# Optimization experiments

Measured on AMD Instinct MI355X. Metric: run time of the kernel, lower is better.

## Reference

```python
import jax, jax.numpy as jnp
import numpy as np

HIDDEN = 1024
MOE_INTER = 512
SHARED_INTER = 2048
N_EXPERTS = 32
TOP_K = 6
N_GROUP = 8
TOPK_GROUP = 4
ROUTED_SCALE = 2.5


def setup_inputs() -> dict:
    key = jax.random.key(0)
    ks = jax.random.split(key, 6)
    s = 0.02
    return {
        "hidden_states": jax.random.normal(ks[0], (2, 1024, HIDDEN), jnp.float32),
        "gate_w": jax.random.normal(ks[1], (N_EXPERTS, HIDDEN), jnp.float32) * s,
        "e_bias": jnp.zeros((N_EXPERTS,), jnp.float32),  # e_score_correction_bias (non-trainable)
        "up_w": jax.random.normal(ks[2], (N_EXPERTS, MOE_INTER, HIDDEN), jnp.float32) * s,
        "down_w": jax.random.normal(ks[3], (N_EXPERTS, HIDDEN, MOE_INTER), jnp.float32) * s,
        "shared_up_w": jax.random.normal(ks[4], (SHARED_INTER, HIDDEN), jnp.float32) * s,
        "shared_down_w": jax.random.normal(ks[5], (HIDDEN, SHARED_INTER), jnp.float32) * s,
    }


def _relu2(x):
    # Nemotron-H 'relu2' activation: relu(x)^2
    return jnp.square(jax.nn.relu(x))


def _router(x, gate_w, e_bias):
    # x: [T, H] -> topk_idx [T, K] (int), topk_w [T, K] (fp32)
    T = x.shape[0]
    logits = x.astype(jnp.float32) @ gate_w.astype(jnp.float32).T  # [T, E]
    scores = jax.nn.sigmoid(logits)
    sc = scores + e_bias[None, :]
    # group-limited routing: top-2 sum per group, keep topk_group groups
    g = sc.reshape(T, N_GROUP, N_EXPERTS // N_GROUP)
    group_scores = jax.lax.top_k(g, 2)[0].sum(-1)                  # [T, G]
    group_idx = jax.lax.top_k(group_scores, TOPK_GROUP)[1]         # [T, TG]
    group_mask = jnp.zeros_like(group_scores).at[jnp.arange(T)[:, None], group_idx].set(1.0)
    score_mask = jnp.repeat(group_mask, N_EXPERTS // N_GROUP, axis=1)  # [T, E]
    masked = jnp.where(score_mask > 0, sc, 0.0)
    topk_idx = jax.lax.stop_gradient(jax.lax.top_k(masked, TOP_K)[1])  # torch path is @no_grad
    topk_w = jnp.take_along_axis(scores, topk_idx, axis=1)         # gather from unbiased scores
    topk_w = topk_w / (topk_w.sum(-1, keepdims=True) + 1e-20)      # norm_topk_prob
    topk_w = topk_w * ROUTED_SCALE
    return topk_idx, topk_w


def reference(hidden_states, gate_w, e_bias, up_w, down_w, shared_up_w, shared_down_w):
    B, S, H = hidden_states.shape
    x = hidden_states.reshape(-1, H)  # [T, H]
    T = x.shape[0]
    topk_idx, topk_w = _router(x, gate_w, e_bias)
    # combine weights as dense [T, E] (scatter of top-k weights)
    combine = jnp.zeros((T, N_EXPERTS), topk_w.dtype).at[jnp.arange(T)[:, None], topk_idx].add(topk_w)
    # dense-masked expert compute; weight applied on intermediate (equivalent since
    # down_proj is linear with no bias): out = sum_e w_te * down_e(act(up_e(x)))
    h = _relu2(jnp.einsum('th,eih->tei', x, up_w))   # [T, E, I]
    h = h * combine[:, :, None]
    moe_out = jnp.einsum('tei,ehi->th', h, down_w)   # [T, H]
    shared = _relu2(x @ shared_up_w.T) @ shared_down_w.T
    return (moe_out + shared).reshape(B, S, H)


if __name__ == "__main__":
    out = reference(**setup_inputs())
    print(out.shape, out.dtype)
```

## Files before the change

### kernel.cpp

```cpp
#include <hip/hip_runtime.h>

typedef unsigned short u16;
typedef __bf16 bf16x8 __attribute__((ext_vector_type(8)));
typedef float f32x4 __attribute__((ext_vector_type(4)));
typedef u16 u16x8 __attribute__((ext_vector_type(8)));

#define T_TOK 2048
#define HID   1024
#define NEXP  32
#define IM    512
#define SI    2048
#define TOPK  6
#define PLAN_MAX 160

__device__ __forceinline__ u16 f2bf(float f){
  unsigned u = __float_as_uint(f);
  u += 0x7FFFu + ((u >> 16) & 1u);
  return (u16)(u >> 16);
}

__device__ __forceinline__ void gll16(const void* g, void* l){
  __builtin_amdgcn_global_load_lds((const __attribute__((address_space(1))) void*)g,
                                   (__attribute__((address_space(3))) void*)l, 16, 0, 0);
}

__device__ __forceinline__ u16x8 cvt2(float4 a, float4 b){
  u16x8 o;
  o[0] = f2bf(a.x); o[1] = f2bf(a.y); o[2] = f2bf(a.z); o[3] = f2bf(a.w);
  o[4] = f2bf(b.x); o[5] = f2bf(b.y); o[6] = f2bf(b.z); o[7] = f2bf(b.w);
  return o;
}

__global__ __launch_bounds__(256) void cvt_big_kernel(const float4* __restrict__ s1,
                                                      const float4* __restrict__ s2,
                                                      u16x8* __restrict__ d1,
                                                      u16x8* __restrict__ d2){
  long i = (long)blockIdx.x * 256 + threadIdx.x;
  const float4* s; u16x8* d;
  if (i < 2097152L){ s = s1; d = d1; }
  else             { s = s2; d = d2; i -= 2097152L; }
  float4 a = s[2*i], b = s[2*i+1];
  d[i] = cvt2(a, b);
}

__global__ __launch_bounds__(256) void cvt_small_router_kernel(
    const float* __restrict__ x, const float4* __restrict__ s3, const float4* __restrict__ s4,
    const float* __restrict__ gate, const float* __restrict__ ebias,
    u16x8* __restrict__ d0, u16x8* __restrict__ d3, u16x8* __restrict__ d4,
    int* __restrict__ ce, float* __restrict__ cw){
  int blk = blockIdx.x;
  if (blk >= 512){
    long i = (long)(blk - 512) * 256 + threadIdx.x;
    const float4* s; u16x8* d;
    if      (i < 262144L){ s = (const float4*)x; d = d0; }
    else if (i < 524288L){ s = s3; d = d3; i -= 262144L; }
    else                 { s = s4; d = d4; i -= 524288L; }
    float4 a = s[2*i], b = s[2*i+1];
    d[i] = cvt2(a, b);
    return;
  }
  int wave = threadIdx.x >> 6;
  int lane = threadIdx.x & 63;
  int t = blk * 4 + wave;
  int e = lane & 31, half = lane >> 5;
  const float4* xv = (const float4*)(x + (size_t)t * HID);
  const float4* gv = (const float4*)(gate + (size_t)e * HID);
  double d0a = 0, d1a = 0, d2a = 0, d3a = 0;
  for (int i = half * 128; i < half * 128 + 128; i++){
    float4 a = xv[i], b = gv[i];
    d0a += (double)a.x * b.x; d1a += (double)a.y * b.y;
    d2a += (double)a.z * b.z; d3a += (double)a.w * b.w;
  }
  double acc = (d0a + d1a) + (d2a + d3a);
  acc += __shfl_xor(acc, 32);
  double score = 1.0 / (1.0 + exp(-acc));
  double sc = score + (double)ebias[e];
  double o1  = __shfl_xor(sc, 1);
  double hi  = fmax(sc, o1), lo = fmin(sc, o1);
  double ohi = __shfl_xor(hi, 2), olo = __shfl_xor(lo, 2);
  double gs  = (hi >= ohi) ? hi + fmax(lo, ohi) : ohi + fmax(olo, hi);
  int g = e >> 2;
  int rank = 0;
#pragma unroll
  for (int j = 0; j < 8; j++){
    double gj = __shfl(gs, j * 4);
    if (gj > gs || (gj == gs && j < g)) rank++;
  }
  double cur = (rank < 4) ? sc : 0.0;
  int sel_e[TOPK]; double sel_w[TOPK]; double wsum = 0.0;
#pragma unroll
  for (int k = 0; k < TOPK; k++){
    double bv = cur; int bi = lane;
#pragma unroll
    for (int m = 32; m >= 1; m >>= 1){
      double ov = __shfl_xor(bv, m); int oi = __shfl_xor(bi, m);
      if (ov > bv || (ov == bv && oi < bi)) { bv = ov; bi = oi; }
    }
    if ((bi & 31) == e) cur = -1e300;
    double ws = __shfl(score, bi);
    sel_e[k] = bi; sel_w[k] = ws; wsum += ws;
  }
  double scale = 2.5 / (wsum + 1e-20);
#pragma unroll
  for (int k = 0; k < TOPK; k++){
    if (lane == k){
      ce[t * TOPK + k] = sel_e[k] & 31;
      cw[t * TOPK + k] = (float)(sel_w[k] * scale);
    }
  }
}

__global__ __launch_bounds__(256) void build_kernel(const int* __restrict__ ce,
                                                    const float* __restrict__ cw,
                                                    int* __restrict__ cnt,
                                                    int* __restrict__ tok,
                                                    float* __restrict__ wl){
  int e = blockIdx.x;
  int tid = threadIdx.x, lane = tid & 63, wave = tid >> 6;
  __shared__ int wsum[4];
  int running = 0;
  for (int base = 0; base < T_TOK * TOPK; base += 256){
    int i = base + tid;
    bool m = (ce[i] == e);
    unsigned long long bal = __ballot(m);
    int woff = __popcll(bal & ((1ull << lane) - 1ull));
    if (lane == 0) wsum[wave] = __popcll(bal);
    __syncthreads();
    int wbase = 0;
#pragma unroll
    for (int wv = 0; wv < 4; wv++) if (wv < wave) wbase += wsum[wv];
    int btot = wsum[0] + wsum[1] + wsum[2] + wsum[3];
    if (m){
      int t = i / TOPK, k = i - t * TOPK;
      int pos = running + wbase + woff;
      tok[e * T_TOK + pos] = (t << 3) | k;
      wl[e * T_TOK + pos] = cw[i];
    }
    running += btot;
    __syncthreads();
  }
  if (tid == 0) cnt[e] = running;
}

__global__ __launch_bounds__(256) void plan_kernel(const int* __restrict__ cnt,
                                                   int* __restrict__ plan){
  int tid = threadIdx.x;
  if (tid < PLAN_MAX) plan[1 + tid] = -1;
  __syncthreads();
  if (tid == 0){
    int n = 0;
    for (int e = 0; e < NEXP; e++){
      int c = cnt[e];
      for (int tb = 0; tb < c; tb += 128) plan[1 + n++] = (tb << 8) | e;
    }
    plan[0] = n;
  }
}

__device__ __forceinline__ void gemm_core(
    const char* gA0, const char* gA1, const char* gB0, const char* gB1,
    u16* lA, u16* lB, int iters, int tid, int wrow, int wcol, int quad, int l16,
    f32x4 acc[4][4])
{
  char* bA = (char*)lA + tid*16;
  char* bB = (char*)lB + tid*16;
  gll16(gA0, bA);  gll16(gA1, bA + 4096);
  gll16(gB0, bB);  gll16(gB1, bB + 4096);
  gA0 += 64; gA1 += 64; gB0 += 64; gB1 += 64;
  __syncthreads();
  unsigned cur = 0;
  for (int it = 0; it < iters - 1; ++it){
    unsigned nxt = cur ^ 1;
    gll16(gA0, bA + nxt*8192);  gll16(gA1, bA + nxt*8192 + 4096);
    gll16(gB0, bB + nxt*8192);  gll16(gB1, bB + nxt*8192 + 4096);
    gA0 += 64; gA1 += 64; gB0 += 64; gB1 += 64;
    const u16* rA = lA + cur*4096;
    const u16* rB = lB + cur*4096;
    bf16x8 af[4], bfr[4];
#pragma unroll
    for (int mt = 0; mt < 4; mt++) af[mt]  = *(const bf16x8*)&rA[(wrow + mt*16 + l16)*32 + quad*8];
#pragma unroll
    for (int nt = 0; nt < 4; nt++) bfr[nt] = *(const bf16x8*)&rB[(wcol + nt*16 + l16)*32 + quad*8];
#pragma unroll
    for (int mt = 0; mt < 4; mt++)
#pragma unroll
      for (int nt = 0; nt < 4; nt++)
        acc[mt][nt] = __builtin_amdgcn_mfma_f32_16x16x32_bf16(af[mt], bfr[nt], acc[mt][nt], 0, 0, 0);
    __syncthreads();
    cur = nxt;
  }
  const u16* rA = lA + cur*4096;
  const u16* rB = lB + cur*4096;
  bf16x8 af[4], bfr[4];
#pragma unroll
  for (int mt = 0; mt < 4; mt++) af[mt]  = *(const bf16x8*)&rA[(wrow + mt*16 + l16)*32 + quad*8];
#pragma unroll
  for (int nt = 0; nt < 4; nt++) bfr[nt] = *(const bf16x8*)&rB[(wcol + nt*16 + l16)*32 + quad*8];
#pragma unroll
  for (int mt = 0; mt < 4; mt++)
#pragma unroll
    for (int nt = 0; nt < 4; nt++)
      acc[mt][nt] = __builtin_amdgcn_mfma_f32_16x16x32_bf16(af[mt], bfr[nt], acc[mt][nt], 0, 0, 0);
}

#define ACC_INIT f32x4 acc[4][4]; \
  _Pragma("unroll") for (int i_ = 0; i_ < 4; i_++) \
  _Pragma("unroll") for (int j_ = 0; j_ < 4; j_++) acc[i_][j_] = (f32x4){0.f,0.f,0.f,0.f};

__global__ __launch_bounds__(256) void up_fused_kernel(
    const u16* __restrict__ xb, const u16* __restrict__ supb, const u16* __restrict__ upb,
    const int* __restrict__ cnt, const int* __restrict__ tok, const float* __restrict__ wl,
    const int* __restrict__ plan, u16* __restrict__ shh, u16* __restrict__ hws){
  __shared__ u16 lA[2*128*32], lB[2*128*32];
  int tid = threadIdx.x;
  int lane = tid & 63, wave = tid >> 6, quad = lane >> 4, l16 = lane & 15;
  int wrow = (wave >> 1)*64, wcol = (wave & 1)*64;
  int srow = tid >> 2, sseg = (tid & 3)*16;
  int blk = blockIdx.x;
  if (blk < 256){
    int bm = (blk >> 4) * 128, bn = (blk & 15) * 128;
    const char* gA0 = (const char*)(xb + (size_t)(bm + srow)*HID) + sseg;
    const char* gA1 = (const char*)(xb + (size_t)(bm + 64 + srow)*HID) + sseg;
    const char* gB0 = (const char*)(supb + (size_t)(bn + srow)*HID) + sseg;
    const char* gB1 = (const char*)(supb + (size_t)(bn + 64 + srow)*HID) + sseg;
    ACC_INIT;
    gemm_core(gA0, gA1, gB0, gB1, lA, lB, HID/32, tid, wrow, wcol, quad, l16, acc);
#pragma unroll
    for (int mt = 0; mt < 4; mt++)
#pragma unroll
      for (int nt = 0; nt < 4; nt++)
#pragma unroll
        for (int r = 0; r < 4; r++){
          int m = bm + wrow + mt*16 + quad*4 + r;
          int n = bn + wcol + nt*16 + l16;
          float v = acc[mt][nt][r]; v = fmaxf(v, 0.f); v *= v;
          shh[(size_t)m*SI + n] = f2bf(v);
        }
  } else {
    int eu = blk - 256;
    int pv = plan[1 + (eu >> 2)];
    if (pv < 0) return;
    int e = pv & 255;
    int tb = pv >> 8;
    int c = cnt[e];
    int bn = (eu & 3) * 128;
    const int* tl = tok + e * T_TOK;
    const float* wle = wl + e * T_TOK;
    int s0 = tb + srow;      if (s0 > c-1) s0 = c-1;
    int s1 = tb + 64 + srow; if (s1 > c-1) s1 = c-1;
    int t0 = tl[s0] >> 3, t1 = tl[s1] >> 3;
    const char* gA0 = (const char*)(xb + (size_t)t0*HID) + sseg;
    const char* gA1 = (const char*)(xb + (size_t)t1*HID) + sseg;
    const u16* Bb = upb + (size_t)e * IM * HID;
    const char* gB0 = (const char*)(Bb + (size_t)(bn + srow)*HID) + sseg;
    const char* gB1 = (const char*)(Bb + (size_t)(bn + 64 + srow)*HID) + sseg;
    ACC_INIT;
    gemm_core(gA0, gA1, gB0, gB1, lA, lB, HID/32, tid, wrow, wcol, quad, l16, acc);
#pragma unroll
    for (int mt = 0; mt < 4; mt++)
#pragma unroll
      for (int r = 0; r < 4; r++){
        int s = tb + wrow + mt*16 + quad*4 + r;
        if (s < c){
          int code = tl[s];
          float w = wle[s];
          size_t hb = ((size_t)(code >> 3) * TOPK + (code & 7)) * IM;
#pragma unroll
          for (int nt = 0; nt < 4; nt++){
            float v = acc[mt][nt][r]; v = fmaxf(v, 0.f); v = v * v * w;
            hws[hb + bn + wcol + nt*16 + l16] = f2bf(v);
          }
        }
      }
  }
}

__global__ __launch_bounds__(256) void down_fused_kernel(
    const u16* __restrict__ shh, const u16* __restrict__ sdnb,
    const u16* __restrict__ hws, const u16* __restrict__ dnb,
    const int* __restrict__ cnt, const int* __restrict__ tok, const int* __restrict__ plan,
    float* __restrict__ out){
  __shared__ u16 lA[2*128*32], lB[2*128*32];
  int tid = threadIdx.x;
  int lane = tid & 63, wave = tid >> 6, quad = lane >> 4, l16 = lane & 15;
  int wrow = (wave >> 1)*64, wcol = (wave & 1)*64;
  int srow = tid >> 2, sseg = (tid & 3)*16;
  int blk = blockIdx.x;
  if (blk < 128){
    int bm = (blk >> 3)*128, bn = (blk & 7)*128;
    const char* gA0 = (const char*)(shh + (size_t)(bm + srow)*SI) + sseg;
    const char* gA1 = (const char*)(shh + (size_t)(bm + 64 + srow)*SI) + sseg;
    const char* gB0 = (const char*)(sdnb + (size_t)(bn + srow)*SI) + sseg;
    const char* gB1 = (const char*)(sdnb + (size_t)(bn + 64 + srow)*SI) + sseg;
    ACC_INIT;
    gemm_core(gA0, gA1, gB0, gB1, lA, lB, SI/32, tid, wrow, wcol, quad, l16, acc);
#pragma unroll
    for (int mt = 0; mt < 4; mt++)
#pragma unroll
      for (int nt = 0; nt < 4; nt++)
#pragma unroll
        for (int r = 0; r < 4; r++){
          int m = bm + wrow + mt*16 + quad*4 + r;
          int n = bn + wcol + nt*16 + l16;
          unsafeAtomicAdd(&out[(size_t)m*HID + n], acc[mt][nt][r]);
        }
  } else {
    int eu = blk - 128;
    int pv = plan[1 + (eu >> 3)];
    if (pv < 0) return;
    int e = pv & 255;
    int tb = pv >> 8;
    int c = cnt[e];
    int bn = (eu & 7) * 128;
    const int* tl = tok + e * T_TOK;
    int s0 = tb + srow;      if (s0 > c-1) s0 = c-1;
    int s1 = tb + 64 + srow; if (s1 > c-1) s1 = c-1;
    int c0 = tl[s0], c1 = tl[s1];
    const char* gA0 = (const char*)(hws + ((size_t)(c0 >> 3)*TOPK + (c0 & 7))*IM) + sseg;
    const char* gA1 = (const char*)(hws + ((size_t)(c1 >> 3)*TOPK + (c1 & 7))*IM) + sseg;
    const u16* Bb = dnb + (size_t)e * HID * IM;
    const char* gB0 = (const char*)(Bb + (size_t)(bn + srow)*IM) + sseg;
    const char* gB1 = (const char*)(Bb + (size_t)(bn + 64 + srow)*IM) + sseg;
    ACC_INIT;
    gemm_core(gA0, gA1, gB0, gB1, lA, lB, IM/32, tid, wrow, wcol, quad, l16, acc);
#pragma unroll
    for (int mt = 0; mt < 4; mt++)
#pragma unroll
      for (int r = 0; r < 4; r++){
        int s = tb + wrow + mt*16 + quad*4 + r;
        if (s < c){
          int code = tl[s];
          float* ob = out + (size_t)(code >> 3) * HID;
#pragma unroll
          for (int nt = 0; nt < 4; nt++)
            unsafeAtomicAdd(&ob[bn + wcol + nt*16 + l16], acc[mt][nt][r]);
        }
      }
  }
}

extern "C" void kernel_launch(void* const* d_in, const int* in_sizes, int n_in,
                              void* d_out, int out_size, void* d_ws, size_t ws_size,
                              hipStream_t stream) {
  const float* x    = (const float*)d_in[0];
  const float* gate = (const float*)d_in[1];
  const float* eb   = (const float*)d_in[2];
  const float* upw  = (const float*)d_in[3];
  const float* dnw  = (const float*)d_in[4];
  const float* supw = (const float*)d_in[5];
  const float* sdnw = (const float*)d_in[6];
  float* out = (float*)d_out;

  char* w = (char*)d_ws;
  size_t o = 0;
  int*   cnt  = (int*)(w + o);   o += 1024;
  int*   plan = (int*)(w + o);   o += 1024;
  int*   ce   = (int*)(w + o);   o += (size_t)T_TOK * TOPK * 4;
  float* cw   = (float*)(w + o); o += (size_t)T_TOK * TOPK * 4;
  int*   tok  = (int*)(w + o);   o += (size_t)NEXP * T_TOK * 4;
  float* wl   = (float*)(w + o); o += (size_t)NEXP * T_TOK * 4;
  u16*   xb   = (u16*)(w + o);   o += (size_t)T_TOK * HID * 2;
  u16*   dnb  = (u16*)(w + o);   o += (size_t)NEXP * HID * IM * 2;
  u16*   hws  = (u16*)(w + o);   o += (size_t)T_TOK * TOPK * IM * 2;
  u16*   upb  = (u16*)(w + o);   o += (size_t)NEXP * IM * HID * 2;
  u16*   supb = (u16*)(w + o);   o += (size_t)SI * HID * 2;
  u16*   sdnb = (u16*)(w + o);   o += (size_t)HID * SI * 2;
  u16*   shh  = (u16*)(w + o);   o += (size_t)T_TOK * SI * 2;

  cvt_big_kernel<<<16384, 256, 0, stream>>>(
      (const float4*)upw, (const float4*)dnw, (u16x8*)upb, (u16x8*)dnb);
  cvt_small_router_kernel<<<3584, 256, 0, stream>>>(
      x, (const float4*)supw, (const float4*)sdnw, gate, eb,
      (u16x8*)xb, (u16x8*)supb, (u16x8*)sdnb, ce, cw);
  build_kernel<<<NEXP, 256, 0, stream>>>(ce, cw, cnt, tok, wl);
  plan_kernel<<<1, 256, 0, stream>>>(cnt, plan);

  up_fused_kernel<<<896, 256, 0, stream>>>(xb, supb, upb, cnt, tok, wl, plan, shh, hws);
  hipMemsetAsync(out, 0, (size_t)T_TOK * HID * 4, stream);
  down_fused_kernel<<<1408, 256, 0, stream>>>(shh, sdnb, hws, dnb, cnt, tok, plan, out);
}
```

Measured before the change: 369.6 us.

## Merge prep kernels, fold plan into build, swizzle LDS, split-K shared down GEMM

```diff
diff --git a/kernel.cpp b/kernel.cpp
--- a/kernel.cpp
+++ b/kernel.cpp
@@ -31,30 +31,27 @@
   return o;
 }
 
-__global__ __launch_bounds__(256) void cvt_big_kernel(const float4* __restrict__ s1,
-                                                      const float4* __restrict__ s2,
-                                                      u16x8* __restrict__ d1,
-                                                      u16x8* __restrict__ d2){
-  long i = (long)blockIdx.x * 256 + threadIdx.x;
-  const float4* s; u16x8* d;
-  if (i < 2097152L){ s = s1; d = d1; }
-  else             { s = s2; d = d2; i -= 2097152L; }
-  float4 a = s[2*i], b = s[2*i+1];
-  d[i] = cvt2(a, b);
-}
-
-__global__ __launch_bounds__(256) void cvt_small_router_kernel(
-    const float* __restrict__ x, const float4* __restrict__ s3, const float4* __restrict__ s4,
+__global__ __launch_bounds__(256) void prep_kernel(
+    const float* __restrict__ x, const float4* __restrict__ upw, const float4* __restrict__ dnw,
+    const float4* __restrict__ supw, const float4* __restrict__ sdnw,
     const float* __restrict__ gate, const float* __restrict__ ebias,
-    u16x8* __restrict__ d0, u16x8* __restrict__ d3, u16x8* __restrict__ d4,
-    int* __restrict__ ce, float* __restrict__ cw){
+    u16x8* __restrict__ xb, u16x8* __restrict__ upb, u16x8* __restrict__ dnb,
+    u16x8* __restrict__ supb, u16x8* __restrict__ sdnb,
+    int* __restrict__ ce, float* __restrict__ cw, int* __restrict__ done){
   int blk = blockIdx.x;
+  if (blk == 0 && threadIdx.x == 0) *done = 0;
   if (blk >= 512){
-    long i = (long)(blk - 512) * 256 + threadIdx.x;
-    const float4* s; u16x8* d;
-    if      (i < 262144L){ s = (const float4*)x; d = d0; }
-    else if (i < 524288L){ s = s3; d = d3; i -= 262144L; }
-    else                 { s = s4; d = d4; i -= 524288L; }
+    const float4* s; u16x8* d; long i;
+    if (blk < 16896){
+      i = (long)(blk - 512) * 256 + threadIdx.x;
+      if (i < 2097152L){ s = upw; d = upb; }
+      else             { s = dnw; d = dnb; i -= 2097152L; }
+    } else {
+      i = (long)(blk - 16896) * 256 + threadIdx.x;
+      if      (i < 262144L){ s = (const float4*)x; d = xb; }
+      else if (i < 524288L){ s = supw; d = supb; i -= 262144L; }
+      else                 { s = sdnw; d = sdnb; i -= 524288L; }
+    }
     float4 a = s[2*i], b = s[2*i+1];
     d[i] = cvt2(a, b);
     return;
@@ -110,14 +107,17 @@
   }
 }
 
-__global__ __launch_bounds__(256) void build_kernel(const int* __restrict__ ce,
-                                                    const float* __restrict__ cw,
-                                                    int* __restrict__ cnt,
-                                                    int* __restrict__ tok,
-                                                    float* __restrict__ wl){
+__global__ __launch_bounds__(256) void build_plan_kernel(const int* __restrict__ ce,
+                                                         const float* __restrict__ cw,
+                                                         int* __restrict__ cnt,
+                                                         int* __restrict__ tok,
+                                                         float* __restrict__ wl,
+                                                         int* __restrict__ done,
+                                                         int* __restrict__ plan){
   int e = blockIdx.x;
   int tid = threadIdx.x, lane = tid & 63, wave = tid >> 6;
   __shared__ int wsum[4];
+  __shared__ int lastflag;
   int running = 0;
   for (int base = 0; base < T_TOK * TOPK; base += 256){
     int i = base + tid;
@@ -139,27 +139,30 @@
     running += btot;
     __syncthreads();
   }
-  if (tid == 0) cnt[e] = running;
-}
-
-__global__ __launch_bounds__(256) void plan_kernel(const int* __restrict__ cnt,
-                                                   int* __restrict__ plan){
-  int tid = threadIdx.x;
-  if (tid < PLAN_MAX) plan[1 + tid] = -1;
+  if (tid == 0){
+    atomicExch(&cnt[e], running);
+    __threadfence();
+    lastflag = (atomicAdd(done, 1) == NEXP - 1);
+  }
   __syncthreads();
-  if (tid == 0){
-    int n = 0;
-    for (int e = 0; e < NEXP; e++){
-      int c = cnt[e];
-      for (int tb = 0; tb < c; tb += 128) plan[1 + n++] = (tb << 8) | e;
-    }
-    plan[0] = n;
+  if (lastflag){
+    __threadfence();
+    if (tid < PLAN_MAX) plan[1 + tid] = -1;
+    __syncthreads();
+    if (tid == 0){
+      int n = 0;
+      for (int ee = 0; ee < NEXP; ee++){
+        int c = (ee == e) ? running : cnt[ee];
+        for (int tb = 0; tb < c; tb += 128) plan[1 + n++] = (tb << 8) | ee;
+      }
+      plan[0] = n;
+    }
   }
 }
 
 __device__ __forceinline__ void gemm_core(
     const char* gA0, const char* gA1, const char* gB0, const char* gB1,
-    u16* lA, u16* lB, int iters, int tid, int wrow, int wcol, int quad, int l16,
+    u16* lA, u16* lB, int iters, int tid, int wrow, int wcol, int qsw, int l16,
     f32x4 acc[4][4])
 {
   char* bA = (char*)lA + tid*16;
@@ -178,9 +181,9 @@
     const u16* rB = lB + cur*4096;
     bf16x8 af[4], bfr[4];
 #pragma unroll
-    for (int mt = 0; mt < 4; mt++) af[mt]  = *(const bf16x8*)&rA[(wrow + mt*16 + l16)*32 + quad*8];
-#pragma unroll
-    for (int nt = 0; nt < 4; nt++) bfr[nt] = *(const bf16x8*)&rB[(wcol + nt*16 + l16)*32 + quad*8];
+    for (int mt = 0; mt < 4; mt++) af[mt]  = *(const bf16x8*)&rA[(wrow + mt*16 + l16)*32 + qsw*8];
+#pragma unroll
+    for (int nt = 0; nt < 4; nt++) bfr[nt] = *(const bf16x8*)&rB[(wcol + nt*16 + l16)*32 + qsw*8];
 #pragma unroll
     for (int mt = 0; mt < 4; mt++)
 #pragma unroll
@@ -193,9 +196,9 @@
   const u16* rB = lB + cur*4096;
   bf16x8 af[4], bfr[4];
 #pragma unroll
-  for (int mt = 0; mt < 4; mt++) af[mt]  = *(const bf16x8*)&rA[(wrow + mt*16 + l16)*32 + quad*8];
-#pragma unroll
-  for (int nt = 0; nt < 4; nt++) bfr[nt] = *(const bf16x8*)&rB[(wcol + nt*16 + l16)*32 + quad*8];
+  for (int mt = 0; mt < 4; mt++) af[mt]  = *(const bf16x8*)&rA[(wrow + mt*16 + l16)*32 + qsw*8];
+#pragma unroll
+  for (int nt = 0; nt < 4; nt++) bfr[nt] = *(const bf16x8*)&rB[(wcol + nt*16 + l16)*32 + qsw*8];
 #pragma unroll
   for (int mt = 0; mt < 4; mt++)
 #pragma unroll
@@ -206,16 +209,20 @@
 #define ACC_INIT f32x4 acc[4][4]; \
   _Pragma("unroll") for (int i_ = 0; i_ < 4; i_++) \
   _Pragma("unroll") for (int j_ = 0; j_ < 4; j_++) acc[i_][j_] = (f32x4){0.f,0.f,0.f,0.f};
+
+#define GEO_INIT int tid = threadIdx.x; \
+  int lane = tid & 63, wave = tid >> 6, quad = lane >> 4, l16 = lane & 15; \
+  int wrow = (wave >> 1)*64, wcol = (wave & 1)*64; \
+  int srow = tid >> 2; \
+  int sseg = ((tid & 3) ^ ((tid >> 3) & 3)) * 16; \
+  int qsw  = quad ^ ((l16 >> 1) & 3);
 
 __global__ __launch_bounds__(256) void up_fused_kernel(
     const u16* __restrict__ xb, const u16* __restrict__ supb, const u16* __restrict__ upb,
     const int* __restrict__ cnt, const int* __restrict__ tok, const float* __restrict__ wl,
     const int* __restrict__ plan, u16* __restrict__ shh, u16* __restrict__ hws){
   __shared__ u16 lA[2*128*32], lB[2*128*32];
-  int tid = threadIdx.x;
-  int lane = tid & 63, wave = tid >> 6, quad = lane >> 4, l16 = lane & 15;
-  int wrow = (wave >> 1)*64, wcol = (wave & 1)*64;
-  int srow = tid >> 2, sseg = (tid & 3)*16;
+  GEO_INIT;
   int blk = blockIdx.x;
   if (blk < 256){
     int bm = (blk >> 4) * 128, bn = (blk & 15) * 128;
@@ -224,7 +231,7 @@
     const char* gB0 = (const char*)(supb + (size_t)(bn + srow)*HID) + sseg;
     const char* gB1 = (const char*)(supb + (size_t)(bn + 64 + srow)*HID) + sseg;
     ACC_INIT;
-    gemm_core(gA0, gA1, gB0, gB1, lA, lB, HID/32, tid, wrow, wcol, quad, l16, acc);
+    gemm_core(gA0, gA1, gB0, gB1, lA, lB, HID/32, tid, wrow, wcol, qsw, l16, acc);
 #pragma unroll
     for (int mt = 0; mt < 4; mt++)
 #pragma unroll
@@ -255,7 +262,7 @@
     const char* gB0 = (const char*)(Bb + (size_t)(bn + srow)*HID) + sseg;
     const char* gB1 = (const char*)(Bb + (size_t)(bn + 64 + srow)*HID) + sseg;
     ACC_INIT;
-    gemm_core(gA0, gA1, gB0, gB1, lA, lB, HID/32, tid, wrow, wcol, quad, l16, acc);
+    gemm_core(gA0, gA1, gB0, gB1, lA, lB, HID/32, tid, wrow, wcol, qsw, l16, acc);
 #pragma unroll
     for (int mt = 0; mt < 4; mt++)
 #pragma unroll
@@ -281,19 +288,18 @@
     const int* __restrict__ cnt, const int* __restrict__ tok, const int* __restrict__ plan,
     float* __restrict__ out){
   __shared__ u16 lA[2*128*32], lB[2*128*32];
-  int tid = threadIdx.x;
-  int lane = tid & 63, wave = tid >> 6, quad = lane >> 4, l16 = lane & 15;
-  int wrow = (wave >> 1)*64, wcol = (wave & 1)*64;
-  int srow = tid >> 2, sseg = (tid & 3)*16;
+  GEO_INIT;
   int blk = blockIdx.x;
-  if (blk < 128){
-    int bm = (blk >> 3)*128, bn = (blk & 7)*128;
-    const char* gA0 = (const char*)(shh + (size_t)(bm + srow)*SI) + sseg;
-    const char* gA1 = (const char*)(shh + (size_t)(bm + 64 + srow)*SI) + sseg;
-    const char* gB0 = (const char*)(sdnb + (size_t)(bn + srow)*SI) + sseg;
-    const char* gB1 = (const char*)(sdnb + (size_t)(bn + 64 + srow)*SI) + sseg;
+  if (blk < 512){
+    int kc = blk & 3;
+    int bn = ((blk >> 2) & 7) * 128;
+    int bm = (blk >> 5) * 128;
+    const char* gA0 = (const char*)(shh + (size_t)(bm + srow)*SI + kc*512) + sseg;
+    const char* gA1 = (const char*)(shh + (size_t)(bm + 64 + srow)*SI + kc*512) + sseg;
+    const char* gB0 = (const char*)(sdnb + (size_t)(bn + srow)*SI + kc*512) + sseg;
+    const char* gB1 = (const char*)(sdnb + (size_t)(bn + 64 + srow)*SI + kc*512) + sseg;
     ACC_INIT;
-    gemm_core(gA0, gA1, gB0, gB1, lA, lB, SI/32, tid, wrow, wcol, quad, l16, acc);
+    gemm_core(gA0, gA1, gB0, gB1, lA, lB, 16, tid, wrow, wcol, qsw, l16, acc);
 #pragma unroll
     for (int mt = 0; mt < 4; mt++)
 #pragma unroll
@@ -305,7 +311,7 @@
           unsafeAtomicAdd(&out[(size_t)m*HID + n], acc[mt][nt][r]);
         }
   } else {
-    int eu = blk - 128;
+    int eu = blk - 512;
     int pv = plan[1 + (eu >> 3)];
     if (pv < 0) return;
     int e = pv & 255;
@@ -322,7 +328,7 @@
     const char* gB0 = (const char*)(Bb + (size_t)(bn + srow)*IM) + sseg;
     const char* gB1 = (const char*)(Bb + (size_t)(bn + 64 + srow)*IM) + sseg;
     ACC_INIT;
-    gemm_core(gA0, gA1, gB0, gB1, lA, lB, IM/32, tid, wrow, wcol, quad, l16, acc);
+    gemm_core(gA0, gA1, gB0, gB1, lA, lB, IM/32, tid, wrow, wcol, qsw, l16, acc);
 #pragma unroll
     for (int mt = 0; mt < 4; mt++)
 #pragma unroll
@@ -366,16 +372,14 @@
   u16*   supb = (u16*)(w + o);   o += (size_t)SI * HID * 2;
   u16*   sdnb = (u16*)(w + o);   o += (size_t)HID * SI * 2;
   u16*   shh  = (u16*)(w + o);   o += (size_t)T_TOK * SI * 2;
-
-  cvt_big_kernel<<<16384, 256, 0, stream>>>(
-      (const float4*)upw, (const float4*)dnw, (u16x8*)upb, (u16x8*)dnb);
-  cvt_small_router_kernel<<<3584, 256, 0, stream>>>(
-      x, (const float4*)supw, (const float4*)sdnw, gate, eb,
-      (u16x8*)xb, (u16x8*)supb, (u16x8*)sdnb, ce, cw);
-  build_kernel<<<NEXP, 256, 0, stream>>>(ce, cw, cnt, tok, wl);
-  plan_kernel<<<1, 256, 0, stream>>>(cnt, plan);
-
+  int*   done = cnt + 32;
+
+  hipMemsetAsync(out, 0, (size_t)T_TOK * HID * 4, stream);
+  prep_kernel<<<19968, 256, 0, stream>>>(
+      x, (const float4*)upw, (const float4*)dnw, (const float4*)supw, (const float4*)sdnw,
+      gate, eb, (u16x8*)xb, (u16x8*)upb, (u16x8*)dnb, (u16x8*)supb, (u16x8*)sdnb,
+      ce, cw, done);
+  build_plan_kernel<<<NEXP, 256, 0, stream>>>(ce, cw, cnt, tok, wl, done, plan);
   up_fused_kernel<<<896, 256, 0, stream>>>(xb, supb, upb, cnt, tok, wl, plan, shh, hws);
-  hipMemsetAsync(out, 0, (size_t)T_TOK * HID * 4, stream);
-  down_fused_kernel<<<1408, 256, 0, stream>>>(shh, sdnb, hws, dnb, cnt, tok, plan, out);
-}
+  down_fused_kernel<<<1792, 256, 0, stream>>>(shh, sdnb, hws, dnb, cnt, tok, plan, out);
+}
```

After: 360.0 us. -2.6%, faster.
